# Optimization experiments

Measured on AMD Instinct MI355X. Metric: run time of the kernel, lower is better.

Reference implementation:

```python
import jax, jax.numpy as jnp
import numpy as np

B, T, C = 2, 2048, 2048
H, D, G = 16, 128, 4   # num_heads, head_dim, num_kv_groups
EPS = 1e-6


def setup_inputs() -> dict:
    key = jax.random.key(0)
    ks = jax.random.split(key, 6)
    x = jax.random.normal(ks[0], (B, T, C), dtype=jnp.float32)
    # causal mask: True = disallowed (strictly upper triangular)
    mask = jnp.triu(jnp.ones((T, T), dtype=bool), k=1)
    # RoPE tables, full head_dim with duplicated angle halves
    inv_freq = 1.0 / (10000.0 ** (jnp.arange(0, D, 2, dtype=jnp.float32) / D))
    angles = jnp.arange(T, dtype=jnp.float32)[:, None] * inv_freq[None, :]  # [T, D/2]
    angles = jnp.concatenate([angles, angles], axis=-1)                     # [T, D]
    cos, sin = jnp.cos(angles), jnp.sin(angles)
    std = 0.02
    W_query = jax.random.normal(ks[1], (C, H * D), dtype=jnp.float32) * std
    W_key = jax.random.normal(ks[2], (C, G * D), dtype=jnp.float32) * std
    W_value = jax.random.normal(ks[3], (C, G * D), dtype=jnp.float32) * std
    W_out = jax.random.normal(ks[4], (H * D, C), dtype=jnp.float32) * std
    q_scale = jnp.ones((D,), dtype=jnp.float32)
    k_scale = jnp.ones((D,), dtype=jnp.float32)
    return {"x": x, "mask": mask, "cos": cos, "sin": sin,
            "W_query": W_query, "W_key": W_key, "W_value": W_value,
            "W_out": W_out, "q_scale": q_scale, "k_scale": k_scale}


def _rmsnorm(x, scale):
    # qwen3-compatible: compute in fp32, rescale, cast back
    xf = x.astype(jnp.float32)
    var = jnp.mean(xf * xf, axis=-1, keepdims=True)
    return (xf * jax.lax.rsqrt(var + EPS) * scale).astype(x.dtype)


def _rope(x, cos, sin):
    d = x.shape[-1]
    x1, x2 = x[..., : d // 2], x[..., d // 2 :]
    rotated = jnp.concatenate([-x2, x1], axis=-1)
    # cos/sin: [T, D] -> broadcast over [B, H, T, D]
    return (x * cos[None, None] + rotated * sin[None, None]).astype(x.dtype)


def reference(x, mask, cos, sin, W_query, W_key, W_value, W_out, q_scale, k_scale):
    b, t, _ = x.shape
    Q = (x @ W_query).reshape(b, t, H, D).transpose(0, 2, 1, 3)  # [B,H,T,D]
    K = (x @ W_key).reshape(b, t, G, D).transpose(0, 2, 1, 3)    # [B,G,T,D]
    V = (x @ W_value).reshape(b, t, G, D).transpose(0, 2, 1, 3)
    group_size = H // G
    K = jnp.repeat(K, group_size, axis=1)  # [B,H,T,D]
    V = jnp.repeat(V, group_size, axis=1)
    Q = _rmsnorm(Q, q_scale)
    K = _rmsnorm(K, k_scale)
    Q = _rope(Q, cos, sin)
    K = _rope(K, cos, sin)
    scale = D ** (-0.5)
    attn = jnp.einsum("bhqd,bhkd->bhqk", Q, K) * scale
    attn = jnp.where(mask[None, None], -jnp.inf, attn)
    w = jax.nn.softmax(attn, axis=-1)
    out = jnp.einsum("bhqk,bhkd->bhqd", w, V)
    out = out.transpose(0, 2, 1, 3).reshape(b, t, H * D)
    return out @ W_out
```

## Files before the change

### kernel.cpp

```cpp
#include <hip/hip_runtime.h>
#include <hip/hip_bf16.h>

#define Bq 2
#define Tt 2048
#define Cc 2048
#define Hh 16
#define Dd 128
#define Gg 4

using bf16 = __hip_bfloat16;
typedef __attribute__((ext_vector_type(8))) short short8;
typedef __attribute__((ext_vector_type(4))) float f32x4;

__device__ __forceinline__ void gload_lds16(const void* g, void* l) {
    __builtin_amdgcn_global_load_lds(
        (const __attribute__((address_space(1))) unsigned int*)g,
        (__attribute__((address_space(3))) unsigned int*)l, 16, 0, 0);
}

__global__ void k_cast_bf16(const float* __restrict__ in, bf16* __restrict__ out, int n4) {
    int i = blockIdx.x * blockDim.x + threadIdx.x;
    if (i >= n4) return;
    float4 v = ((const float4*)in)[i];
    union { bf16 h[4]; uint2 u; } u;
    u.h[0] = __float2bfloat16(v.x);
    u.h[1] = __float2bfloat16(v.y);
    u.h[2] = __float2bfloat16(v.z);
    u.h[3] = __float2bfloat16(v.w);
    ((uint2*)out)[i] = u.u;
}

__global__ void k_cast_transpose(const float* __restrict__ in, bf16* __restrict__ out,
                                 int rows, int cols, int ostride) {
    __shared__ float tile[32][33];
    int c0 = blockIdx.x * 32, r0 = blockIdx.y * 32;
    int tx = threadIdx.x, ty = threadIdx.y;
    #pragma unroll
    for (int k = 0; k < 4; ++k)
        tile[ty + 8*k][tx] = in[(size_t)(r0 + ty + 8*k) * cols + c0 + tx];
    __syncthreads();
    #pragma unroll
    for (int k = 0; k < 4; ++k)
        out[(size_t)(c0 + ty + 8*k) * ostride + r0 + tx] = __float2bfloat16(tile[tx][ty + 8*k]);
}

__global__ void k_vt(const bf16* __restrict__ QKV, bf16* __restrict__ Vt) {
    __shared__ bf16 tile[64][65];
    const int d0 = blockIdx.x * 64, t0 = blockIdx.y * 64;
    const int bg = blockIdx.z;
    const int b = bg >> 2, g = bg & 3;
    const int tx = threadIdx.x, ty = threadIdx.y;
    const bf16* src = QKV + (size_t)(b * Tt) * 3072 + 2560 + g * 128;
    #pragma unroll
    for (int k = 0; k < 8; ++k)
        tile[ty + 8*k][tx] = src[(size_t)(t0 + ty + 8*k) * 3072 + d0 + tx];
    __syncthreads();
    bf16* dst = Vt + (size_t)bg * Dd * Tt;
    #pragma unroll
    for (int k = 0; k < 8; ++k)
        dst[(size_t)(d0 + ty + 8*k) * Tt + t0 + tx] = tile[tx][ty + 8*k];
}

template<int OUTF32>
__global__ __launch_bounds__(256)
void k_gemm_bt(const bf16* __restrict__ A, const bf16* __restrict__ Bt,
               void* __restrict__ C, int M, int N, int K) {
    __shared__ __align__(16) bf16 As[128 * 64];
    __shared__ __align__(16) bf16 Bs[128 * 64];
    const int lane = threadIdx.x & 63;
    const int wave = threadIdx.x >> 6;
    const int row0 = blockIdx.y * 128;
    const int col0 = blockIdx.x * 128;
    const int wm = wave >> 1, wn = wave & 1;
    f32x4 acc[4][4] = {};

    const int srow = lane >> 3;
    const int schunk = ((lane & 7) ^ srow) * 8;

    for (int k0 = 0; k0 < K; k0 += 64) {
        #pragma unroll
        for (int j = 0; j < 4; ++j) {
            const int c = j * 4 + wave;
            const int rt = c * 8 + srow;
            gload_lds16(A  + (size_t)(row0 + rt) * K + k0 + schunk, As + c * 512);
            gload_lds16(Bt + (size_t)(col0 + rt) * K + k0 + schunk, Bs + c * 512);
        }
        __syncthreads();
        #pragma unroll
        for (int kk = 0; kk < 2; ++kk) {
            short8 af[4], bfr[4];
            #pragma unroll
            for (int i = 0; i < 4; ++i) {
                const int ra = wm * 64 + i * 16 + (lane & 15);
                af[i] = *(const short8*)((const char*)As + ra * 128 +
                        ((kk * 64 + (lane >> 4) * 16) ^ ((ra & 7) << 4)));
                const int rb = wn * 64 + i * 16 + (lane & 15);
                bfr[i] = *(const short8*)((const char*)Bs + rb * 128 +
                        ((kk * 64 + (lane >> 4) * 16) ^ ((rb & 7) << 4)));
            }
            __builtin_amdgcn_s_setprio(1);
            #pragma unroll
            for (int i = 0; i < 4; ++i)
                #pragma unroll
                for (int j = 0; j < 4; ++j)
                    acc[i][j] = __builtin_amdgcn_mfma_f32_16x16x32_bf16(af[i], bfr[j], acc[i][j], 0, 0, 0);
            __builtin_amdgcn_s_setprio(0);
        }
        __syncthreads();
    }

    const int crow0 = row0 + wm * 64 + (lane >> 4) * 4;
    const int ccol0 = col0 + wn * 64 + (lane & 15);
    #pragma unroll
    for (int i = 0; i < 4; ++i)
        #pragma unroll
        for (int j = 0; j < 4; ++j)
            #pragma unroll
            for (int r = 0; r < 4; ++r) {
                const size_t idx = (size_t)(crow0 + i * 16 + r) * N + ccol0 + j * 16;
                const float v = acc[i][j][r];
                if (OUTF32) ((float*)C)[idx] = v;
                else        ((bf16*)C)[idx] = __float2bfloat16(v);
            }
}

__global__ void k_qkv_post(const bf16* __restrict__ QKV,
                           const float* __restrict__ cosT, const float* __restrict__ sinT,
                           const float* __restrict__ qs, const float* __restrict__ ks,
                           bf16* __restrict__ Qr, bf16* __restrict__ Kr) {
    const int bt = blockIdx.x;
    const int b = bt >> 11;
    const int t = bt & 2047;
    const int lane = threadIdx.x & 63;
    const int wave = threadIdx.x >> 6;
    const float c1 = cosT[t * 128 + lane],      c2 = cosT[t * 128 + 64 + lane];
    const float s1 = sinT[t * 128 + lane],      s2 = sinT[t * 128 + 64 + lane];
    const float qs1 = qs[lane], qs2 = qs[lane + 64];
    const float ks1 = ks[lane], ks2 = ks[lane + 64];
    const bf16* rowb = QKV + (size_t)bt * 3072;
    for (int rr = wave; rr < 20; rr += 4) {
        const bf16* src = rowb + rr * 128;
        const float x1 = __bfloat162float(src[lane]);
        const float x2 = __bfloat162float(src[lane + 64]);
        bf16* dst;
        if (rr < 16) dst = Qr + ((size_t)(b * Hh + rr) * Tt + t) * 128;
        else         dst = Kr + ((size_t)(b * Gg + (rr - 16)) * Tt + t) * 128;
        float ssum = x1 * x1 + x2 * x2;
        #pragma unroll
        for (int o = 32; o > 0; o >>= 1) ssum += __shfl_xor(ssum, o);
        const float inv = rsqrtf(ssum * (1.0f / 128.0f) + 1e-6f);
        const float post = (rr < 16) ? 0.08838834764831845f : 1.0f;
        const float sc1 = ((rr < 16) ? qs1 : ks1) * inv;
        const float sc2 = ((rr < 16) ? qs2 : ks2) * inv;
        const float y1 = x1 * sc1;
        const float y2 = x2 * sc2;
        dst[lane]      = __float2bfloat16((y1 * c1 - y2 * s1) * post);
        dst[lane + 64] = __float2bfloat16((y2 * c2 + y1 * s2) * post);
    }
}

__global__ __launch_bounds__(256)
void k_attn(const bf16* __restrict__ Qr, const bf16* __restrict__ Kr,
            const bf16* __restrict__ Vt, bf16* __restrict__ AO) {
    __shared__ __align__(16) bf16 Ksm[2][64 * 128];
    __shared__ __align__(16) bf16 Vsm[2][128 * 64];
    __shared__ __align__(16) bf16 Psm[4][16 * 64];
    const int id = blockIdx.x;
    const int bg = id & 7;
    const int wid = id >> 3;
    const int pair = wid & 15;
    const int hg = wid >> 4;
    const int b = bg >> 2, g = bg & 3;
    const int h = g * 4 + hg;
    const int lane = threadIdx.x & 63;
    const int wave = threadIdx.x >> 6;

    const bf16* Kbase = Kr + (size_t)(b * Gg + g) * Tt * Dd;
    const bf16* Vbase = Vt + (size_t)(b * Gg + g) * Dd * Tt;

    for (int pass = 0; pass < 2; ++pass) {
        const int qt = pass ? (31 - pair) : pair;
        const bf16* Qbase = Qr + ((size_t)(b * Hh + h) * Tt + qt * 64) * Dd;

        short8 qf[4];
        #pragma unroll
        for (int kk = 0; kk < 4; ++kk)
            qf[kk] = *(const short8*)(Qbase + (size_t)(wave * 16 + (lane & 15)) * 128 + kk * 32 + (lane >> 4) * 8);

        float l_run[4] = {0.f, 0.f, 0.f, 0.f};
        f32x4 oacc[8];
        #pragma unroll
        for (int j = 0; j < 8; ++j) oacc[j] = (f32x4){0.f, 0.f, 0.f, 0.f};

        {
            #pragma unroll
            for (int j = 0; j < 4; ++j) {
                const int c = j * 4 + wave;
                const int rtk = c * 4 + (lane >> 4);
                const int chk = (lane & 15) ^ (rtk & 7);
                gload_lds16(Kbase + (size_t)rtk * 128 + chk * 8, Ksm[0] + c * 512);
                const int rtv = c * 8 + (lane >> 3);
                const int chv = (lane & 7) ^ ((lane >> 3) & 7);
                gload_lds16(Vbase + (size_t)rtv * Tt + chv * 8, Vsm[0] + c * 512);
            }
        }

        int cur = 0;
        for (int tk = 0; tk <= qt; ++tk) {
            __syncthreads();

            if (tk < qt) {
                const int k0n = (tk + 1) * 64;
                #pragma unroll
                for (int j = 0; j < 4; ++j) {
                    const int c = j * 4 + wave;
                    const int rtk = c * 4 + (lane >> 4);
                    const int chk = (lane & 15) ^ (rtk & 7);
                    gload_lds16(Kbase + (size_t)(k0n + rtk) * 128 + chk * 8, Ksm[cur ^ 1] + c * 512);
                    const int rtv = c * 8 + (lane >> 3);
                    const int chv = (lane & 7) ^ ((lane >> 3) & 7);
                    gload_lds16(Vbase + (size_t)rtv * Tt + k0n + chv * 8, Vsm[cur ^ 1] + c * 512);
                }
            }

            const bf16* Ks = Ksm[cur];
            const bf16* Vs = Vsm[cur];

            f32x4 s[4];
            #pragma unroll
            for (int nt = 0; nt < 4; ++nt) s[nt] = (f32x4){0.f, 0.f, 0.f, 0.f};
            __builtin_amdgcn_s_setprio(1);
            #pragma unroll
            for (int nt = 0; nt < 4; ++nt) {
                #pragma unroll
                for (int kk = 0; kk < 4; ++kk) {
                    const int rk = nt * 16 + (lane & 15);
                    short8 kf = *(const short8*)((const char*)Ks + rk * 256 +
                                ((kk * 64 + (lane >> 4) * 16) ^ ((rk & 7) << 4)));
                    s[nt] = __builtin_amdgcn_mfma_f32_16x16x32_bf16(qf[kk], kf, s[nt], 0, 0, 0);
                }
            }
            __builtin_amdgcn_s_setprio(0);

            if (tk == qt) {
                const int qrow = qt * 64 + wave * 16 + (lane >> 4) * 4;
                const int k0 = tk * 64;
                #pragma unroll
                for (int nt = 0; nt < 4; ++nt) {
                    const int kcol = k0 + nt * 16 + (lane & 15);
                    #pragma unroll
                    for (int r = 0; r < 4; ++r)
                        if (kcol > qrow + r) s[nt][r] = -1e30f;
                }
            }

            #pragma unroll
            for (int nt = 0; nt < 4; ++nt)
                #pragma unroll
                for (int r = 0; r < 4; ++r) {
                    const float p = __expf(s[nt][r]);
                    l_run[r] += p;
                    s[nt][r] = p;
                }

            #pragma unroll
            for (int nt = 0; nt < 4; ++nt)
                #pragma unroll
                for (int r = 0; r < 4; ++r) {
                    const int prow = (lane >> 4) * 4 + r;
                    const int pcol = nt * 16 + (lane & 15);
                    *(bf16*)((char*)Psm[wave] + ((prow * 128 + pcol * 2) ^ ((prow & 7) << 4))) =
                        __float2bfloat16(s[nt][r]);
                }
            #pragma unroll
            for (int kk = 0; kk < 2; ++kk) {
                const int pr = lane & 15;
                short8 pf = *(const short8*)((const char*)Psm[wave] + pr * 128 +
                            ((kk * 64 + (lane >> 4) * 16) ^ ((pr & 7) << 4)));
                __builtin_amdgcn_s_setprio(1);
                #pragma unroll
                for (int j = 0; j < 8; ++j) {
                    const int rb = j * 16 + (lane & 15);
                    short8 vf = *(const short8*)((const char*)Vs + rb * 128 +
                                ((kk * 64 + (lane >> 4) * 16) ^ ((rb & 7) << 4)));
                    oacc[j] = __builtin_amdgcn_mfma_f32_16x16x32_bf16(pf, vf, oacc[j], 0, 0, 0);
                }
                __builtin_amdgcn_s_setprio(0);
            }
            cur ^= 1;
        }
        __syncthreads();

        #pragma unroll
        for (int o = 1; o < 16; o <<= 1)
            #pragma unroll
            for (int r = 0; r < 4; ++r) l_run[r] += __shfl_xor(l_run[r], o);

        #pragma unroll
        for (int r = 0; r < 4; ++r) {
            const float inv = 1.0f / l_run[r];
            const int qrow = qt * 64 + wave * 16 + (lane >> 4) * 4 + r;
            bf16* dst = AO + (size_t)(b * Tt + qrow) * 2048 + h * 128 + (lane & 15);
            #pragma unroll
            for (int j = 0; j < 8; ++j)
                dst[j * 16] = __float2bfloat16(oacc[j][r] * inv);
        }
    }
}

extern "C" void kernel_launch(void* const* d_in, const int* in_sizes, int n_in,
                              void* d_out, int out_size, void* d_ws, size_t ws_size,
                              hipStream_t stream) {
    const float* x    = (const float*)d_in[0];
    const float* cosT = (const float*)d_in[2];
    const float* sinT = (const float*)d_in[3];
    const float* Wq   = (const float*)d_in[4];
    const float* Wk   = (const float*)d_in[5];
    const float* Wv   = (const float*)d_in[6];
    const float* Wo   = (const float*)d_in[7];
    const float* qs   = (const float*)d_in[8];
    const float* ks   = (const float*)d_in[9];

    char* ws = (char*)d_ws;
    bf16* xb   = (bf16*)(ws);
    bf16* Wcat = (bf16*)(ws + 16777216);
    bf16* Wot  = (bf16*)(ws + 29360128);
    bf16* QKV  = (bf16*)(ws + 37748736);
    bf16* Qr   = (bf16*)(ws + 62914560);
    bf16* Kr   = (bf16*)(ws + 79691776);
    bf16* Vtp  = (bf16*)(ws + 83886080);
    bf16* AO   = (bf16*)(ws + 88080384);

    k_cast_bf16<<<8192, 256, 0, stream>>>(x, xb, 2097152);
    dim3 tb(32, 8);
    k_cast_transpose<<<dim3(64, 64), tb, 0, stream>>>(Wq, Wcat, 2048, 2048, 2048);
    k_cast_transpose<<<dim3(16, 64), tb, 0, stream>>>(Wk, Wcat + (size_t)2048 * 2048, 2048, 512, 2048);
    k_cast_transpose<<<dim3(16, 64), tb, 0, stream>>>(Wv, Wcat + (size_t)2560 * 2048, 2048, 512, 2048);
    k_cast_transpose<<<dim3(64, 64), tb, 0, stream>>>(Wo, Wot, 2048, 2048, 2048);

    k_gemm_bt<0><<<dim3(24, 32), 256, 0, stream>>>(xb, Wcat, QKV, 4096, 3072, 2048);
    k_qkv_post<<<4096, 256, 0, stream>>>(QKV, cosT, sinT, qs, ks, Qr, Kr);
    k_vt<<<dim3(2, 32, 8), dim3(64, 8), 0, stream>>>(QKV, Vtp);
    k_attn<<<512, 256, 0, stream>>>(Qr, Kr, Vtp, AO);
    k_gemm_bt<1><<<dim3(16, 32), 256, 0, stream>>>(AO, Wot, d_out, 4096, 2048, 2048);
}
```

Before: 199.3 us.

## Add 256x256-tile 8-wave GEMM with quarter-staged pipelining for QKV projection

Adds a new GEMM kernel for the QKV projection that uses a 256x256 output tile with 512 threads. It stages A and B in four 128-row quarter tiles, double buffered, and interleaves the next tile's async LDS loads with MFMA on the current quarters using explicit vmcnt waits and barriers. Blocks are remapped in an XCD-aware order. The larger tile raises reuse per loaded byte and hides load latency, but it uses more LDS and registers per block and launches only 192 blocks, about one wave of blocks on the GPU. The attention loop bounds are reworded without changing behaviour.

After: 199.7 us. No clear change (+0.2%).

```diff
diff --git a/kernel.cpp b/kernel.cpp
--- a/kernel.cpp
+++ b/kernel.cpp
@@ -17,6 +17,8 @@
         (const __attribute__((address_space(1))) unsigned int*)g,
         (__attribute__((address_space(3))) unsigned int*)l, 16, 0, 0);
 }
+
+#define MEMBAR() asm volatile("" ::: "memory")
 
 __global__ void k_cast_bf16(const float* __restrict__ in, bf16* __restrict__ out, int n4) {
     int i = blockIdx.x * blockDim.x + threadIdx.x;
@@ -59,6 +61,155 @@
     #pragma unroll
     for (int k = 0; k < 8; ++k)
         dst[(size_t)(d0 + ty + 8*k) * Tt + t0 + tx] = tile[tx][ty + 8*k];
+}
+
+template<int OUTF32>
+__global__ __launch_bounds__(512, 2)
+void k_gemm256(const bf16* __restrict__ A, const bf16* __restrict__ Bt,
+               void* __restrict__ C, int M, int N, int K, int nbx) {
+    __shared__ __align__(16) bf16 Ls[2][4][128 * 64];
+    const int tid = threadIdx.x;
+    const int lane = tid & 63;
+    const int wid = tid >> 6;
+    const int wm = wid >> 2, wn = wid & 3;
+
+    const int nb = gridDim.x;
+    const int cpx = nb >> 3;
+    const int id = blockIdx.x;
+    const int sid = (id & 7) * cpx + (id >> 3);
+    const int bx = sid % nbx, by = sid / nbx;
+    const int row0 = by * 256, col0 = bx * 256;
+
+    const int NT = K >> 6;
+    f32x4 acc[2][4][2][2] = {};
+
+#define STAGE_HT(bufq, tt, ht) {                                               \
+        const bool isB_ = ((ht) == 1 || (ht) == 2);                            \
+        const int half_ = ((ht) >= 2) ? 128 : 0;                               \
+        _Pragma("unroll")                                                      \
+        for (int c_ = 0; c_ < 2; ++c_) {                                       \
+            const int r_ = c_ * 64 + (tid >> 3);                               \
+            const int ch_ = (tid & 7) ^ (r_ & 7);                              \
+            const bf16* gs_ = (isB_ ? Bt + (size_t)(col0 + half_ + r_) * K     \
+                                    : A  + (size_t)(row0 + half_ + r_) * K)    \
+                              + (tt) * 64 + ch_ * 8;                           \
+            gload_lds16(gs_, &Ls[bufq][ht][c_ * 4096] + tid * 8);              \
+        } }
+
+    STAGE_HT(0, 0, 0); STAGE_HT(0, 0, 1); STAGE_HT(0, 0, 2); STAGE_HT(0, 0, 3);
+
+    for (int t = 0; t < NT; ++t) {
+        const int p = t & 1, q = p ^ 1;
+        const bool pf = (t + 1 < NT);
+        const bf16* hA0 = Ls[p][0];
+        const bf16* hB0 = Ls[p][1];
+        const bf16* hB1 = Ls[p][2];
+        const bf16* hA1 = Ls[p][3];
+
+        short8 af[4][2], bb0[2][2], bb1[2][2];
+
+        auto rdA = [&](const bf16* hh, int i, int kk) -> short8 {
+            const int ra = wm * 64 + i * 16 + (lane & 15);
+            return *(const short8*)((const char*)hh + ra * 128 +
+                   ((kk * 64 + (lane >> 4) * 16) ^ ((ra & 7) << 4)));
+        };
+        auto rdB = [&](const bf16* hh, int j, int kk) -> short8 {
+            const int rb = wn * 32 + j * 16 + (lane & 15);
+            return *(const short8*)((const char*)hh + rb * 128 +
+                   ((kk * 64 + (lane >> 4) * 16) ^ ((rb & 7) << 4)));
+        };
+
+        if (pf) { STAGE_HT(q, t + 1, 0); asm volatile("s_waitcnt vmcnt(6)" ::: "memory"); }
+        else    { asm volatile("s_waitcnt vmcnt(4)" ::: "memory"); }
+        __builtin_amdgcn_s_barrier(); MEMBAR();
+        #pragma unroll
+        for (int i = 0; i < 4; ++i)
+            #pragma unroll
+            for (int kk = 0; kk < 2; ++kk) af[i][kk] = rdA(hA0, i, kk);
+        #pragma unroll
+        for (int j = 0; j < 2; ++j)
+            #pragma unroll
+            for (int kk = 0; kk < 2; ++kk) bb0[j][kk] = rdB(hB0, j, kk);
+        __builtin_amdgcn_s_setprio(1);
+        #pragma unroll
+        for (int i = 0; i < 4; ++i)
+            #pragma unroll
+            for (int j = 0; j < 2; ++j)
+                #pragma unroll
+                for (int kk = 0; kk < 2; ++kk)
+                    acc[0][i][0][j] = __builtin_amdgcn_mfma_f32_16x16x32_bf16(af[i][kk], bb0[j][kk], acc[0][i][0][j], 0, 0, 0);
+        __builtin_amdgcn_s_setprio(0);
+
+        MEMBAR();
+        if (pf) { STAGE_HT(q, t + 1, 1); asm volatile("s_waitcnt vmcnt(6)" ::: "memory"); }
+        else    { asm volatile("s_waitcnt vmcnt(2)" ::: "memory"); }
+        __builtin_amdgcn_s_barrier(); MEMBAR();
+        #pragma unroll
+        for (int j = 0; j < 2; ++j)
+            #pragma unroll
+            for (int kk = 0; kk < 2; ++kk) bb1[j][kk] = rdB(hB1, j, kk);
+        __builtin_amdgcn_s_setprio(1);
+        #pragma unroll
+        for (int i = 0; i < 4; ++i)
+            #pragma unroll
+            for (int j = 0; j < 2; ++j)
+                #pragma unroll
+                for (int kk = 0; kk < 2; ++kk)
+                    acc[0][i][1][j] = __builtin_amdgcn_mfma_f32_16x16x32_bf16(af[i][kk], bb1[j][kk], acc[0][i][1][j], 0, 0, 0);
+        __builtin_amdgcn_s_setprio(0);
+
+        MEMBAR();
+        if (pf) { STAGE_HT(q, t + 1, 2); asm volatile("s_waitcnt vmcnt(6)" ::: "memory"); }
+        else    { asm volatile("s_waitcnt vmcnt(0)" ::: "memory"); }
+        __builtin_amdgcn_s_barrier(); MEMBAR();
+        #pragma unroll
+        for (int i = 0; i < 4; ++i)
+            #pragma unroll
+            for (int kk = 0; kk < 2; ++kk) af[i][kk] = rdA(hA1, i, kk);
+        __builtin_amdgcn_s_setprio(1);
+        #pragma unroll
+        for (int i = 0; i < 4; ++i)
+            #pragma unroll
+            for (int j = 0; j < 2; ++j)
+                #pragma unroll
+                for (int kk = 0; kk < 2; ++kk)
+                    acc[1][i][1][j] = __builtin_amdgcn_mfma_f32_16x16x32_bf16(af[i][kk], bb1[j][kk], acc[1][i][1][j], 0, 0, 0);
+        __builtin_amdgcn_s_setprio(0);
+
+        MEMBAR();
+        if (pf) STAGE_HT(q, t + 1, 3);
+        __builtin_amdgcn_s_setprio(1);
+        #pragma unroll
+        for (int i = 0; i < 4; ++i)
+            #pragma unroll
+            for (int j = 0; j < 2; ++j)
+                #pragma unroll
+                for (int kk = 0; kk < 2; ++kk)
+                    acc[1][i][0][j] = __builtin_amdgcn_mfma_f32_16x16x32_bf16(af[i][kk], bb0[j][kk], acc[1][i][0][j], 0, 0, 0);
+        __builtin_amdgcn_s_setprio(0);
+        MEMBAR();
+        __builtin_amdgcn_s_barrier();
+        MEMBAR();
+    }
+#undef STAGE_HT
+
+    #pragma unroll
+    for (int mh = 0; mh < 2; ++mh)
+        #pragma unroll
+        for (int i = 0; i < 4; ++i)
+            #pragma unroll
+            for (int nh = 0; nh < 2; ++nh)
+                #pragma unroll
+                for (int j = 0; j < 2; ++j)
+                    #pragma unroll
+                    for (int r = 0; r < 4; ++r) {
+                        const int crow = row0 + mh * 128 + wm * 64 + i * 16 + (lane >> 4) * 4 + r;
+                        const int ccol = col0 + nh * 128 + wn * 32 + j * 16 + (lane & 15);
+                        const size_t idx = (size_t)crow * N + ccol;
+                        const float v = acc[mh][i][nh][j][r];
+                        if (OUTF32) ((float*)C)[idx] = v;
+                        else        ((bf16*)C)[idx] = __float2bfloat16(v);
+                    }
 }
 
 template<int OUTF32>
@@ -206,10 +357,11 @@
         }
 
         int cur = 0;
-        for (int tk = 0; tk <= qt; ++tk) {
+        const int nkv = qt + 1;
+        for (int tk = 0; tk < nkv; ++tk) {
             __syncthreads();
 
-            if (tk < qt) {
+            if (tk + 1 < nkv) {
                 const int k0n = (tk + 1) * 64;
                 #pragma unroll
                 for (int j = 0; j < 4; ++j) {
@@ -242,7 +394,7 @@
             }
             __builtin_amdgcn_s_setprio(0);
 
-            if (tk == qt) {
+            if (tk == nkv - 1) {
                 const int qrow = qt * 64 + wave * 16 + (lane >> 4) * 4;
                 const int k0 = tk * 64;
                 #pragma unroll
@@ -338,7 +490,7 @@
     k_cast_transpose<<<dim3(16, 64), tb, 0, stream>>>(Wv, Wcat + (size_t)2560 * 2048, 2048, 512, 2048);
     k_cast_transpose<<<dim3(64, 64), tb, 0, stream>>>(Wo, Wot, 2048, 2048, 2048);
 
-    k_gemm_bt<0><<<dim3(24, 32), 256, 0, stream>>>(xb, Wcat, QKV, 4096, 3072, 2048);
+    k_gemm256<0><<<192, 512, 0, stream>>>(xb, Wcat, QKV, 4096, 3072, 2048, 12);
     k_qkv_post<<<4096, 256, 0, stream>>>(QKV, cosT, sinT, qs, ks, Qr, Kr);
     k_vt<<<dim3(2, 32, 8), dim3(64, 8), 0, stream>>>(QKV, Vtp);
     k_attn<<<512, 256, 0, stream>>>(Qr, Kr, Vtp, AO);
```
